# Optimization experiments

Hardware: AMD Instinct MI355X
Metric: run time of the kernel (lower is better)

Reference implementation:

```python
import jax, jax.numpy as jnp
import numpy as np

N = 20000          # nodes
E = 320000         # edges (avg degree 16)
D_IN, D1, D2, D_OUT = 256, 512, 256, 64
EPS = 1e-5


def _glorot(key, shape):
    lim = (6.0 / (shape[0] + shape[1])) ** 0.5
    return jax.random.uniform(key, shape, jnp.float32, -lim, lim)


def setup_inputs() -> dict:
    key = jax.random.key(0)
    ks = jax.random.split(key, 8)
    x = jax.random.normal(ks[0], (N, D_IN), jnp.float32)
    edge_index = jax.random.randint(ks[1], (2, E), 0, N, dtype=jnp.int64)
    return {
        "x": x,
        "edge_index": edge_index,
        # SAGEConv 1 (SoftmaxAggregation temperature t1 over inp_dim channels)
        "t1": jnp.ones((1, D_IN), jnp.float32),
        "Wl1": _glorot(ks[2], (D_IN, D1)), "bl1": jnp.zeros((D1,), jnp.float32),
        "Wr1": _glorot(ks[3], (D_IN, D1)),
        "g1": jnp.ones((D1,), jnp.float32), "beta1": jnp.zeros((D1,), jnp.float32),
        # SAGEConv 2
        "t2": jnp.ones((1, D1), jnp.float32),
        "Wl2": _glorot(ks[4], (D1, D2)), "bl2": jnp.zeros((D2,), jnp.float32),
        "Wr2": _glorot(ks[5], (D1, D2)),
        "g2": jnp.ones((D2,), jnp.float32), "beta2": jnp.zeros((D2,), jnp.float32),
        # final linear + LayerNorm
        "Wf": _glorot(ks[6], (D2, D_OUT)), "bf": jnp.zeros((D_OUT,), jnp.float32),
        "gx": jnp.ones((D_OUT,), jnp.float32), "betax": jnp.zeros((D_OUT,), jnp.float32),
    }


def _sage_softmax(x, src, dst, t, Wl, bl, Wr, n):
    """SAGEConv with learnable per-channel SoftmaxAggregation."""
    m = x[src]                                              # [E, C] gathered messages
    a = m * t                                               # scaled logits
    amax = jax.ops.segment_max(a, dst, num_segments=n)      # [N, C]
    e = jnp.exp(a - amax[dst])
    denom = jax.ops.segment_sum(e, dst, num_segments=n)     # [N, C]
    w = e / denom[dst]                                      # segment softmax weights
    agg = jax.ops.segment_sum(m * w, dst, num_segments=n)   # weighted neighbor sum
    return agg @ Wl + bl + x @ Wr


def _graph_ln(x, g, b):
    # PyG LayerNorm mode='graph', batch=None: normalize over ALL nodes & channels
    mu = x.mean()
    std = jnp.sqrt(((x - mu) ** 2).mean())
    return (x - mu) / (std + EPS) * g + b


def _ln(x, g, b):
    mu = x.mean(-1, keepdims=True)
    var = ((x - mu) ** 2).mean(-1, keepdims=True)
    return (x - mu) / jnp.sqrt(var + EPS) * g + b


def reference(x, edge_index, t1, Wl1, bl1, Wr1, g1, beta1,
              t2, Wl2, bl2, Wr2, g2, beta2, Wf, bf, gx, betax):
    src, dst = edge_index[0], edge_index[1]
    h = _sage_softmax(x, src, dst, t1, Wl1, bl1, Wr1, N)
    h = jax.nn.relu(_graph_ln(h, g1, beta1))
    h = _sage_softmax(h, src, dst, t2, Wl2, bl2, Wr2, N)
    h = jax.nn.relu(_graph_ln(h, g2, beta2))
    p = h.mean(0, keepdims=True)                            # global_mean_pool, batch=None -> [1, 256]
    out = _ln(p @ Wf + bf, gx, betax)
    return jax.nn.relu(out)
```

## Files before the change

kernel.cpp:

```cpp
#include <hip/hip_runtime.h>
#include <math.h>

#define NODES 20000
#define MPAD  20096
#define EDGES 320000
#define EPSV  1e-5f
#define LOG2E 1.4426950408889634f

typedef short bf16x8 __attribute__((ext_vector_type(8)));
typedef float f32x4  __attribute__((ext_vector_type(4)));
typedef float f2     __attribute__((ext_vector_type(2)));

__device__ __forceinline__ unsigned short f2bf(float f) {
    unsigned int u = __float_as_uint(f);
    u = (u + 0x7fffu + ((u >> 16) & 1u)) >> 16;
    return (unsigned short)u;
}
__device__ __forceinline__ float bf2f(unsigned short h) {
    return __uint_as_float(((unsigned int)h) << 16);
}

__device__ __forceinline__ void load_lds16(const unsigned short* g, unsigned short* l) {
    __builtin_amdgcn_global_load_lds(
        (const __attribute__((address_space(1))) unsigned int*)g,
        (__attribute__((address_space(3))) unsigned int*)l, 16, 0, 0);
}

__global__ void k_count(const int* __restrict__ dst, int* __restrict__ counts) {
    int e = blockIdx.x * blockDim.x + threadIdx.x;
    if (e < EDGES) atomicAdd(&counts[dst[e]], 1);
}

__global__ void k_scan(const int* __restrict__ counts, int* __restrict__ offs) {
    __shared__ int ssum[256];
    int t = threadIdx.x;
    const int chunk = (NODES + 255) / 256;
    int b = t * chunk, e = b + chunk;
    if (b > NODES) b = NODES;
    if (e > NODES) e = NODES;
    int s = 0;
    for (int i = b; i < e; i++) s += counts[i];
    ssum[t] = s;
    __syncthreads();
    int v = s;
#pragma unroll
    for (int o = 1; o < 256; o <<= 1) {
        int add = (t >= o) ? ssum[t - o] : 0;
        __syncthreads();
        v += add;
        ssum[t] = v;
        __syncthreads();
    }
    int run = v - s;
    if (t == 255) offs[NODES] = v;
    for (int i = b; i < e; i++) { offs[i] = run; run += counts[i]; }
}

__global__ void k_scatter(const int* __restrict__ src, const int* __restrict__ dst,
                          const int* __restrict__ offs, int* __restrict__ cursor,
                          int* __restrict__ csr_src) {
    int e = blockIdx.x * blockDim.x + threadIdx.x;
    if (e < EDGES) {
        int d = dst[e];
        int pos = atomicAdd(&cursor[d], 1);
        csr_src[offs[d] + pos] = src[e];
    }
}

__global__ void k_cast(const float* __restrict__ in, unsigned short* __restrict__ out) {
    int i = (blockIdx.x * blockDim.x + threadIdx.x) * 4;
    float4 v = *(const float4*)(in + i);
    out[i + 0] = f2bf(v.x); out[i + 1] = f2bf(v.y);
    out[i + 2] = f2bf(v.z); out[i + 3] = f2bf(v.w);
}

__global__ void k_transpose_all(const float* __restrict__ Wl1, const float* __restrict__ Wr1,
                                const float* __restrict__ Wl2, const float* __restrict__ Wr2,
                                unsigned short* __restrict__ o1l, unsigned short* __restrict__ o1r,
                                unsigned short* __restrict__ o2l, unsigned short* __restrict__ o2r) {
    __shared__ float tile[32][33];
    int z = blockIdx.z;
    const float* W = (z == 0) ? Wl1 : (z == 1) ? Wr1 : (z == 2) ? Wl2 : Wr2;
    unsigned short* Wt = (z == 0) ? o1l : (z == 1) ? o1r : (z == 2) ? o2l : o2r;
    int K = (z < 2) ? 256 : 512, N = (z < 2) ? 512 : 256;
    int nb = N / 32;
    int n0 = (blockIdx.x % nb) * 32, k0 = (blockIdx.x / nb) * 32;
    int tx = threadIdx.x, ty = threadIdx.y;
#pragma unroll
    for (int j = 0; j < 4; j++)
        tile[ty + j * 8][tx] = W[(size_t)(k0 + ty + j * 8) * N + n0 + tx];
    __syncthreads();
#pragma unroll
    for (int j = 0; j < 4; j++)
        Wt[(size_t)(n0 + ty + j * 8) * K + k0 + tx] = f2bf(tile[tx][ty + j * 8]);
}

template <int C, int S, int UNR>
__global__ void k_agg(const unsigned short* __restrict__ xb, const float* __restrict__ tt,
                      const int* __restrict__ offs, const int* __restrict__ csr,
                      unsigned short* __restrict__ out) {
    constexpr int CS  = C / S;
    constexpr int VPL = CS / 64;
    constexpr int W   = VPL / 2;
    typedef unsigned int uv __attribute__((ext_vector_type(W)));
    typedef unsigned short usv __attribute__((ext_vector_type(VPL)));
    int waveg = (int)((blockIdx.x * (unsigned)blockDim.x + threadIdx.x) >> 6);
    int lane = threadIdx.x & 63;
    int node = waveg / S;
    int slice = waveg % S;
    if (node >= NODES) return;
    int beg = __builtin_amdgcn_readfirstlane(offs[node]);
    int end = __builtin_amdgcn_readfirstlane(offs[node + 1]);
    int cb = slice * CS + lane * VPL;
    const unsigned short* __restrict__ xcb = xb + cb;
    f2 tl[W], l[W], s[W];
#pragma unroll
    for (int i = 0; i < W; i++) {
        tl[i][0] = tt[cb + 2 * i] * LOG2E;
        tl[i][1] = tt[cb + 2 * i + 1] * LOG2E;
        l[i][0] = 0.f; l[i][1] = 0.f;
        s[i][0] = 0.f; s[i][1] = 0.f;
    }
    int k = beg;
    for (; k + UNR <= end; k += UNR) {
        uv v[UNR];
#pragma unroll
        for (int u = 0; u < UNR; u++) {
            int sn = csr[k + u];
            v[u] = *(const uv*)(xcb + (size_t)sn * C);
        }
#pragma unroll
        for (int u = 0; u < UNR; u++)
#pragma unroll
            for (int i = 0; i < W; i++) {
                unsigned wd = v[u][i];
                f2 xv;
                xv[0] = __uint_as_float(wd << 16);
                xv[1] = __uint_as_float(wd & 0xffff0000u);
                f2 a = xv * tl[i];
                f2 p;
                p[0] = __builtin_amdgcn_exp2f(a[0]);
                p[1] = __builtin_amdgcn_exp2f(a[1]);
                l[i] += p;
                s[i] = __builtin_elementwise_fma(p, xv, s[i]);
            }
    }
    for (; k < end; k++) {
        int sn = csr[k];
        uv vv = *(const uv*)(xcb + (size_t)sn * C);
#pragma unroll
        for (int i = 0; i < W; i++) {
            unsigned wd = vv[i];
            f2 xv;
            xv[0] = __uint_as_float(wd << 16);
            xv[1] = __uint_as_float(wd & 0xffff0000u);
            f2 a = xv * tl[i];
            f2 p;
            p[0] = __builtin_amdgcn_exp2f(a[0]);
            p[1] = __builtin_amdgcn_exp2f(a[1]);
            l[i] += p;
            s[i] = __builtin_elementwise_fma(p, xv, s[i]);
        }
    }
    bool has = end > beg;
    usv o;
#pragma unroll
    for (int i = 0; i < W; i++) {
        o[2 * i]     = f2bf(has ? s[i][0] / l[i][0] : 0.f);
        o[2 * i + 1] = f2bf(has ? s[i][1] / l[i][1] : 0.f);
    }
    *(usv*)(out + (size_t)node * C + cb) = o;
}

template <int K, int NT>
__global__ __launch_bounds__(256) void k_gemm_mfma(
    const unsigned short* __restrict__ A1, const unsigned short* __restrict__ B1t,
    const unsigned short* __restrict__ A2, const unsigned short* __restrict__ B2t,
    const float* __restrict__ bias, unsigned short* __restrict__ Co, int M,
    float* __restrict__ stat) {
    __shared__ short As[128 * 32];
    __shared__ short Bs[128 * 32];
    __shared__ float rs[256], rq[256];

    int t = threadIdx.x;
    int m0 = blockIdx.x * 128, n0 = blockIdx.y * 128;
    int wv = t >> 6, lane = t & 63;
    int wm = wv & 1, wn = wv >> 1;
    int lm = lane & 15, quad = lane >> 4;
    int sr = t >> 2;
    int sc8 = (t & 3) * 8;

    f32x4 acc[4][4] = {};

    for (int ph = 0; ph < 2; ph++) {
        const unsigned short* __restrict__ A  = ph ? A2 : A1;
        const unsigned short* __restrict__ Bt = ph ? B2t : B1t;
        for (int k0 = 0; k0 < K; k0 += 32) {
#pragma unroll
            for (int it = 0; it < 2; it++) {
                load_lds16(A  + (size_t)(m0 + it * 64 + sr) * K + k0 + sc8,
                           (unsigned short*)&As[it * 2048 + wv * 512]);
                load_lds16(Bt + (size_t)(n0 + it * 64 + sr) * K + k0 + sc8,
                           (unsigned short*)&Bs[it * 2048 + wv * 512]);
            }
            __syncthreads();
            bf16x8 af[4], bfr[4];
#pragma unroll
            for (int i = 0; i < 4; i++) {
                af[i]  = *(const bf16x8*)&As[(wm * 64 + i * 16 + lm) * 32 + quad * 8];
                bfr[i] = *(const bf16x8*)&Bs[(wn * 64 + i * 16 + lm) * 32 + quad * 8];
            }
#pragma unroll
            for (int mi = 0; mi < 4; mi++)
#pragma unroll
                for (int nj = 0; nj < 4; nj++)
                    acc[mi][nj] = __builtin_amdgcn_mfma_f32_16x16x32_bf16(
                        af[mi], bfr[nj], acc[mi][nj], 0, 0, 0);
            __syncthreads();
        }
    }

    float sum = 0.f, ss = 0.f;
#pragma unroll
    for (int mi = 0; mi < 4; mi++) {
        int rb = m0 + wm * 64 + mi * 16 + quad * 4;
#pragma unroll
        for (int nj = 0; nj < 4; nj++) {
            int col = n0 + wn * 64 + nj * 16 + lm;
            float bb = bias[col];
#pragma unroll
            for (int rg = 0; rg < 4; rg++) {
                int row = rb + rg;
                if (row < M) {
                    float y = acc[mi][nj][rg] + bb;
                    Co[(size_t)row * NT + col] = f2bf(y);
                    sum += y; ss += y * y;
                }
            }
        }
    }
    rs[t] = sum; rq[t] = ss;
    __syncthreads();
    for (int o = 128; o > 0; o >>= 1) {
        if (t < o) { rs[t] += rs[t + o]; rq[t] += rq[t + o]; }
        __syncthreads();
    }
    if (t == 0) { atomicAdd(&stat[0], rs[0]); atomicAdd(&stat[1], rq[0]); }
}

template <int C>
__global__ void k_ln_relu_b(unsigned short* __restrict__ h, int n,
                            const float* __restrict__ st,
                            const float* __restrict__ g, const float* __restrict__ b) {
    typedef unsigned short us8 __attribute__((ext_vector_type(8)));
    float mu = st[0] / (float)n;
    float var = st[1] / (float)n - mu * mu;
    var = var < 0.f ? 0.f : var;
    float inv = 1.0f / (sqrtf(var) + EPSV);
    int i8 = (blockIdx.x * blockDim.x + threadIdx.x) * 8;
    if (i8 >= n) return;
    int c = i8 & (C - 1);
    us8 v = *(const us8*)(h + i8);
    us8 o;
#pragma unroll
    for (int j = 0; j < 8; j++) {
        float y = (bf2f(v[j]) - mu) * inv * g[c + j] + b[c + j];
        o[j] = f2bf(fmaxf(y, 0.f));
    }
    *(us8*)(h + i8) = o;
}

__global__ void k_ln_colsum(const unsigned short* __restrict__ h, int n,
                            const float* __restrict__ st,
                            const float* __restrict__ g, const float* __restrict__ b,
                            float* __restrict__ colsum) {
    float mu = st[0] / (float)n;
    float var = st[1] / (float)n - mu * mu;
    var = var < 0.f ? 0.f : var;
    float inv = 1.0f / (sqrtf(var) + EPSV);
    int t = threadIdx.x;
    float gv = g[t], bv = b[t];
    float local = 0.f;
    int stride = gridDim.x * blockDim.x;
    for (int i = blockIdx.x * blockDim.x + t; i < n; i += stride) {
        float y = (bf2f(h[i]) - mu) * inv * gv + bv;
        local += fmaxf(y, 0.f);
    }
    atomicAdd(&colsum[t], local);
}

__global__ void k_final(const float* __restrict__ colsum, const float* __restrict__ Wf,
                        const float* __restrict__ bf, const float* __restrict__ gx,
                        const float* __restrict__ bx, float* __restrict__ out) {
    __shared__ float p[256];
    int t = threadIdx.x;
    p[t] = colsum[t] * (1.0f / (float)NODES);
    __syncthreads();
    if (t < 64) {
        float acc = bf[t];
        for (int c = 0; c < 256; c++) acc = fmaf(p[c], Wf[c * 64 + t], acc);
        float sum = acc;
        for (int o = 32; o > 0; o >>= 1) sum += __shfl_xor(sum, o);
        float mu = sum * (1.0f / 64.0f);
        float d = acc - mu;
        float vs = d * d;
        for (int o = 32; o > 0; o >>= 1) vs += __shfl_xor(vs, o);
        float var = vs * (1.0f / 64.0f);
        float y = d * rsqrtf(var + EPSV) * gx[t] + bx[t];
        out[t] = fmaxf(y, 0.f);
    }
}

extern "C" void kernel_launch(void* const* d_in, const int* in_sizes, int n_in,
                              void* d_out, int out_size, void* d_ws, size_t ws_size,
                              hipStream_t stream) {
    const float* x   = (const float*)d_in[0];
    const int*   ei  = (const int*)d_in[1];
    const float* t1  = (const float*)d_in[2];
    const float* Wl1 = (const float*)d_in[3];
    const float* bl1 = (const float*)d_in[4];
    const float* Wr1 = (const float*)d_in[5];
    const float* g1  = (const float*)d_in[6];
    const float* be1 = (const float*)d_in[7];
    const float* t2  = (const float*)d_in[8];
    const float* Wl2 = (const float*)d_in[9];
    const float* bl2 = (const float*)d_in[10];
    const float* Wr2 = (const float*)d_in[11];
    const float* g2  = (const float*)d_in[12];
    const float* be2 = (const float*)d_in[13];
    const float* Wf  = (const float*)d_in[14];
    const float* bf  = (const float*)d_in[15];
    const float* gx  = (const float*)d_in[16];
    const float* bx  = (const float*)d_in[17];
    float* out = (float*)d_out;

    char* ws = (char*)d_ws;
    size_t off = 0;
    auto alloc = [&](size_t bytes) { size_t o = off; off = (off + bytes + 511) & ~511ull; return o; };
    size_t o_counts = alloc((size_t)NODES * 4);
    size_t o_cursor = alloc((size_t)NODES * 4);
    size_t o_acc    = alloc(4 * 4);
    size_t o_colsum = alloc(256 * 4);
    size_t zero_bytes = off;
    size_t o_offs = alloc((size_t)(NODES + 1) * 4);
    size_t o_csrc = alloc((size_t)EDGES * 4);
    size_t o_w1l  = alloc((size_t)512 * 256 * 2);
    size_t o_w1r  = alloc((size_t)512 * 256 * 2);
    size_t o_w2l  = alloc((size_t)256 * 512 * 2);
    size_t o_w2r  = alloc((size_t)256 * 512 * 2);
    size_t o_bufX = alloc((size_t)MPAD * 256 * 2);
    size_t o_agg  = alloc((size_t)MPAD * 512 * 2);
    size_t o_h1   = alloc((size_t)MPAD * 512 * 2);

    int*   counts = (int*)(ws + o_counts);
    int*   cursor = (int*)(ws + o_cursor);
    float* acc    = (float*)(ws + o_acc);
    float* colsum = (float*)(ws + o_colsum);
    int*   offs   = (int*)(ws + o_offs);
    int*   csrc   = (int*)(ws + o_csrc);
    unsigned short* w1lt = (unsigned short*)(ws + o_w1l);
    unsigned short* w1rt = (unsigned short*)(ws + o_w1r);
    unsigned short* w2lt = (unsigned short*)(ws + o_w2l);
    unsigned short* w2rt = (unsigned short*)(ws + o_w2r);
    unsigned short* xb   = (unsigned short*)(ws + o_bufX);
    unsigned short* h2p  = (unsigned short*)(ws + o_bufX);
    unsigned short* aggb = (unsigned short*)(ws + o_agg);
    unsigned short* h1   = (unsigned short*)(ws + o_h1);

    const int* src = ei;
    const int* dst = ei + EDGES;

    hipMemsetAsync(ws, 0, zero_bytes, stream);

    k_count<<<(EDGES + 255) / 256, 256, 0, stream>>>(dst, counts);
    k_scan<<<1, 256, 0, stream>>>(counts, offs);
    k_scatter<<<(EDGES + 255) / 256, 256, 0, stream>>>(src, dst, offs, cursor, csrc);
    k_cast<<<NODES * 256 / 4 / 256, 256, 0, stream>>>(x, xb);
    k_transpose_all<<<dim3(128, 1, 4), dim3(32, 8), 0, stream>>>(
        Wl1, Wr1, Wl2, Wr2, w1lt, w1rt, w2lt, w2rt);

    k_agg<256, 2, 8><<<(NODES * 2 + 3) / 4, 256, 0, stream>>>(xb, t1, offs, csrc, aggb);
    k_gemm_mfma<256, 512><<<dim3(MPAD / 128, 4), 256, 0, stream>>>(
        aggb, w1lt, xb, w1rt, bl1, h1, NODES, acc);
    k_ln_relu_b<512><<<NODES * 512 / 8 / 256, 256, 0, stream>>>(h1, NODES * 512, acc, g1, be1);

    k_agg<512, 2, 4><<<(NODES * 2 + 3) / 4, 256, 0, stream>>>(h1, t2, offs, csrc, aggb);
    k_gemm_mfma<512, 256><<<dim3(MPAD / 128, 2), 256, 0, stream>>>(
        aggb, w2lt, h1, w2rt, bl2, h2p, NODES, acc + 2);
    k_ln_colsum<<<1024, 256, 0, stream>>>(h2p, NODES * 256, acc + 2, g2, be2, colsum);

    k_final<<<1, 256, 0, stream>>>(colsum, Wf, bf, gx, bx, out);
}
```

Baseline: 353.6 us.

## Fuse all GNN stages into one persistent cooperative kernel with grid syncs

Replaces the chain of separate kernel launches (CSR build, cast, transpose, two aggregation/GEMM/LN layers, final pooling) with a single cooperative persistent kernel whose stages are separated by grid-wide barriers. The GEMM tiles are reordered in groups of eight M-tiles, and the CSR scatter now counts down the per-node counters instead of using a separate cursor array. The intent is to cut per-launch overhead and inter-kernel gaps. The cost is grid-sync overhead, a grid capped at 1024 blocks with work looped over it, and possible register or occupancy pressure from packing every stage into one kernel.

```diff
diff --git a/kernel.cpp b/kernel.cpp
--- a/kernel.cpp
+++ b/kernel.cpp
@@ -1,5 +1,8 @@
 #include <hip/hip_runtime.h>
+#include <hip/hip_cooperative_groups.h>
 #include <math.h>
+
+namespace cg = cooperative_groups;
 
 #define NODES 20000
 #define MPAD  20096
@@ -26,368 +29,388 @@
         (__attribute__((address_space(3))) unsigned int*)l, 16, 0, 0);
 }
 
-__global__ void k_count(const int* __restrict__ dst, int* __restrict__ counts) {
-    int e = blockIdx.x * blockDim.x + threadIdx.x;
-    if (e < EDGES) atomicAdd(&counts[dst[e]], 1);
-}
-
-__global__ void k_scan(const int* __restrict__ counts, int* __restrict__ offs) {
-    __shared__ int ssum[256];
-    int t = threadIdx.x;
-    const int chunk = (NODES + 255) / 256;
-    int b = t * chunk, e = b + chunk;
-    if (b > NODES) b = NODES;
-    if (e > NODES) e = NODES;
-    int s = 0;
-    for (int i = b; i < e; i++) s += counts[i];
-    ssum[t] = s;
-    __syncthreads();
-    int v = s;
-#pragma unroll
-    for (int o = 1; o < 256; o <<= 1) {
-        int add = (t >= o) ? ssum[t - o] : 0;
-        __syncthreads();
-        v += add;
-        ssum[t] = v;
-        __syncthreads();
-    }
-    int run = v - s;
-    if (t == 255) offs[NODES] = v;
-    for (int i = b; i < e; i++) { offs[i] = run; run += counts[i]; }
-}
-
-__global__ void k_scatter(const int* __restrict__ src, const int* __restrict__ dst,
-                          const int* __restrict__ offs, int* __restrict__ cursor,
-                          int* __restrict__ csr_src) {
-    int e = blockIdx.x * blockDim.x + threadIdx.x;
-    if (e < EDGES) {
-        int d = dst[e];
-        int pos = atomicAdd(&cursor[d], 1);
-        csr_src[offs[d] + pos] = src[e];
-    }
-}
-
-__global__ void k_cast(const float* __restrict__ in, unsigned short* __restrict__ out) {
-    int i = (blockIdx.x * blockDim.x + threadIdx.x) * 4;
-    float4 v = *(const float4*)(in + i);
-    out[i + 0] = f2bf(v.x); out[i + 1] = f2bf(v.y);
-    out[i + 2] = f2bf(v.z); out[i + 3] = f2bf(v.w);
-}
-
-__global__ void k_transpose_all(const float* __restrict__ Wl1, const float* __restrict__ Wr1,
-                                const float* __restrict__ Wl2, const float* __restrict__ Wr2,
-                                unsigned short* __restrict__ o1l, unsigned short* __restrict__ o1r,
-                                unsigned short* __restrict__ o2l, unsigned short* __restrict__ o2r) {
-    __shared__ float tile[32][33];
-    int z = blockIdx.z;
-    const float* W = (z == 0) ? Wl1 : (z == 1) ? Wr1 : (z == 2) ? Wl2 : Wr2;
-    unsigned short* Wt = (z == 0) ? o1l : (z == 1) ? o1r : (z == 2) ? o2l : o2r;
-    int K = (z < 2) ? 256 : 512, N = (z < 2) ? 512 : 256;
-    int nb = N / 32;
-    int n0 = (blockIdx.x % nb) * 32, k0 = (blockIdx.x / nb) * 32;
-    int tx = threadIdx.x, ty = threadIdx.y;
-#pragma unroll
-    for (int j = 0; j < 4; j++)
-        tile[ty + j * 8][tx] = W[(size_t)(k0 + ty + j * 8) * N + n0 + tx];
-    __syncthreads();
-#pragma unroll
-    for (int j = 0; j < 4; j++)
-        Wt[(size_t)(n0 + ty + j * 8) * K + k0 + tx] = f2bf(tile[tx][ty + j * 8]);
-}
+union SMem {
+    struct { short As[128 * 32]; short Bs[128 * 32]; float rs[256]; float rq[256]; } g;
+    float tile[32][33];
+    int   ssum[256];
+    float p[256];
+};
+
+struct Params {
+    const int *src, *dst;
+    const float *x;
+    const float *t1, *bl1, *g1, *be1;
+    const float *t2, *bl2, *g2, *be2;
+    const float *Wl1, *Wr1, *Wl2, *Wr2;
+    const float *Wf, *bf, *gx, *bx;
+    float* out;
+    int *counts, *offs, *csrc;
+    float *acc, *colsum;
+    unsigned short *w1lt, *w1rt, *w2lt, *w2rt;
+    unsigned short *xb, *aggb, *h1, *h2p;
+};
 
 template <int C, int S, int UNR>
-__global__ void k_agg(const unsigned short* __restrict__ xb, const float* __restrict__ tt,
-                      const int* __restrict__ offs, const int* __restrict__ csr,
-                      unsigned short* __restrict__ out) {
+__device__ __forceinline__ void agg_phase(const unsigned short* __restrict__ xb,
+                                          const float* __restrict__ tt,
+                                          const int* __restrict__ offs,
+                                          const int* __restrict__ csr,
+                                          unsigned short* __restrict__ out,
+                                          int gwave, int nwaves) {
     constexpr int CS  = C / S;
     constexpr int VPL = CS / 64;
     constexpr int W   = VPL / 2;
     typedef unsigned int uv __attribute__((ext_vector_type(W)));
     typedef unsigned short usv __attribute__((ext_vector_type(VPL)));
-    int waveg = (int)((blockIdx.x * (unsigned)blockDim.x + threadIdx.x) >> 6);
     int lane = threadIdx.x & 63;
-    int node = waveg / S;
-    int slice = waveg % S;
-    if (node >= NODES) return;
-    int beg = __builtin_amdgcn_readfirstlane(offs[node]);
-    int end = __builtin_amdgcn_readfirstlane(offs[node + 1]);
-    int cb = slice * CS + lane * VPL;
-    const unsigned short* __restrict__ xcb = xb + cb;
-    f2 tl[W], l[W], s[W];
-#pragma unroll
-    for (int i = 0; i < W; i++) {
-        tl[i][0] = tt[cb + 2 * i] * LOG2E;
-        tl[i][1] = tt[cb + 2 * i + 1] * LOG2E;
-        l[i][0] = 0.f; l[i][1] = 0.f;
-        s[i][0] = 0.f; s[i][1] = 0.f;
-    }
-    int k = beg;
-    for (; k + UNR <= end; k += UNR) {
-        uv v[UNR];
-#pragma unroll
-        for (int u = 0; u < UNR; u++) {
-            int sn = csr[k + u];
-            v[u] = *(const uv*)(xcb + (size_t)sn * C);
-        }
-#pragma unroll
-        for (int u = 0; u < UNR; u++)
+    for (int wt = gwave; wt < NODES * S; wt += nwaves) {
+        int node = wt / S, slice = wt % S;
+        int beg = __builtin_amdgcn_readfirstlane(offs[node]);
+        int end = __builtin_amdgcn_readfirstlane(offs[node + 1]);
+        int cb = slice * CS + lane * VPL;
+        const unsigned short* __restrict__ xcb = xb + cb;
+        f2 tl[W], l[W], s[W];
+#pragma unroll
+        for (int i = 0; i < W; i++) {
+            tl[i][0] = tt[cb + 2 * i] * LOG2E;
+            tl[i][1] = tt[cb + 2 * i + 1] * LOG2E;
+            l[i][0] = 0.f; l[i][1] = 0.f;
+            s[i][0] = 0.f; s[i][1] = 0.f;
+        }
+        int k = beg;
+        for (; k + UNR <= end; k += UNR) {
+            uv v[UNR];
+#pragma unroll
+            for (int u = 0; u < UNR; u++) {
+                int sn = csr[k + u];
+                v[u] = *(const uv*)(xcb + (size_t)sn * C);
+            }
+#pragma unroll
+            for (int u = 0; u < UNR; u++)
+#pragma unroll
+                for (int i = 0; i < W; i++) {
+                    unsigned wd = v[u][i];
+                    f2 xv;
+                    xv[0] = __uint_as_float(wd << 16);
+                    xv[1] = __uint_as_float(wd & 0xffff0000u);
+                    f2 a = xv * tl[i];
+                    f2 pp;
+                    pp[0] = __builtin_amdgcn_exp2f(a[0]);
+                    pp[1] = __builtin_amdgcn_exp2f(a[1]);
+                    l[i] += pp;
+                    s[i] = __builtin_elementwise_fma(pp, xv, s[i]);
+                }
+        }
+        for (; k < end; k++) {
+            int sn = csr[k];
+            uv vv = *(const uv*)(xcb + (size_t)sn * C);
 #pragma unroll
             for (int i = 0; i < W; i++) {
-                unsigned wd = v[u][i];
+                unsigned wd = vv[i];
                 f2 xv;
                 xv[0] = __uint_as_float(wd << 16);
                 xv[1] = __uint_as_float(wd & 0xffff0000u);
                 f2 a = xv * tl[i];
-                f2 p;
-                p[0] = __builtin_amdgcn_exp2f(a[0]);
-                p[1] = __builtin_amdgcn_exp2f(a[1]);
-                l[i] += p;
-                s[i] = __builtin_elementwise_fma(p, xv, s[i]);
+                f2 pp;
+                pp[0] = __builtin_amdgcn_exp2f(a[0]);
+                pp[1] = __builtin_amdgcn_exp2f(a[1]);
+                l[i] += pp;
+                s[i] = __builtin_elementwise_fma(pp, xv, s[i]);
             }
-    }
-    for (; k < end; k++) {
-        int sn = csr[k];
-        uv vv = *(const uv*)(xcb + (size_t)sn * C);
+        }
+        bool has = end > beg;
+        usv o;
 #pragma unroll
         for (int i = 0; i < W; i++) {
-            unsigned wd = vv[i];
-            f2 xv;
-            xv[0] = __uint_as_float(wd << 16);
-            xv[1] = __uint_as_float(wd & 0xffff0000u);
-            f2 a = xv * tl[i];
-            f2 p;
-            p[0] = __builtin_amdgcn_exp2f(a[0]);
-            p[1] = __builtin_amdgcn_exp2f(a[1]);
-            l[i] += p;
-            s[i] = __builtin_elementwise_fma(p, xv, s[i]);
-        }
-    }
-    bool has = end > beg;
-    usv o;
-#pragma unroll
-    for (int i = 0; i < W; i++) {
-        o[2 * i]     = f2bf(has ? s[i][0] / l[i][0] : 0.f);
-        o[2 * i + 1] = f2bf(has ? s[i][1] / l[i][1] : 0.f);
-    }
-    *(usv*)(out + (size_t)node * C + cb) = o;
-}
-
-template <int K, int NT>
-__global__ __launch_bounds__(256) void k_gemm_mfma(
+            o[2 * i]     = f2bf(has ? s[i][0] / l[i][0] : 0.f);
+            o[2 * i + 1] = f2bf(has ? s[i][1] / l[i][1] : 0.f);
+        }
+        *(usv*)(out + (size_t)node * C + cb) = o;
+    }
+}
+
+template <int K, int NT, int NTILES>
+__device__ __forceinline__ void gemm_phase(SMem& sm,
     const unsigned short* __restrict__ A1, const unsigned short* __restrict__ B1t,
     const unsigned short* __restrict__ A2, const unsigned short* __restrict__ B2t,
     const float* __restrict__ bias, unsigned short* __restrict__ Co, int M,
     float* __restrict__ stat) {
-    __shared__ short As[128 * 32];
-    __shared__ short Bs[128 * 32];
-    __shared__ float rs[256], rq[256];
-
     int t = threadIdx.x;
-    int m0 = blockIdx.x * 128, n0 = blockIdx.y * 128;
-    int wv = t >> 6, lane = t & 63;
-    int wm = wv & 1, wn = wv >> 1;
-    int lm = lane & 15, quad = lane >> 4;
-    int sr = t >> 2;
-    int sc8 = (t & 3) * 8;
-
-    f32x4 acc[4][4] = {};
-
-    for (int ph = 0; ph < 2; ph++) {
-        const unsigned short* __restrict__ A  = ph ? A2 : A1;
-        const unsigned short* __restrict__ Bt = ph ? B2t : B1t;
-        for (int k0 = 0; k0 < K; k0 += 32) {
-#pragma unroll
-            for (int it = 0; it < 2; it++) {
-                load_lds16(A  + (size_t)(m0 + it * 64 + sr) * K + k0 + sc8,
-                           (unsigned short*)&As[it * 2048 + wv * 512]);
-                load_lds16(Bt + (size_t)(n0 + it * 64 + sr) * K + k0 + sc8,
-                           (unsigned short*)&Bs[it * 2048 + wv * 512]);
+    int G = gridDim.x;
+    constexpr int MH = 20;
+    for (int bx = blockIdx.x; bx < 8 * NTILES * MH; bx += G) {
+        int xid = bx & 7, q = bx >> 3;
+        int n = q % NTILES, mh = q / NTILES;
+        int m = mh * 8 + xid;
+        if (m * 128 >= MPAD) continue;
+        int m0 = m * 128, n0 = n * 128;
+        int wv = t >> 6, lane = t & 63;
+        int wm = wv & 1, wn = wv >> 1;
+        int lm = lane & 15, quad = lane >> 4;
+        int sr = t >> 2;
+        int sc8 = (t & 3) * 8;
+        f32x4 acc[4][4] = {};
+        __syncthreads();
+        for (int ph = 0; ph < 2; ph++) {
+            const unsigned short* __restrict__ A  = ph ? A2 : A1;
+            const unsigned short* __restrict__ Bt = ph ? B2t : B1t;
+            for (int k0 = 0; k0 < K; k0 += 32) {
+#pragma unroll
+                for (int it = 0; it < 2; it++) {
+                    load_lds16(A  + (size_t)(m0 + it * 64 + sr) * K + k0 + sc8,
+                               (unsigned short*)&sm.g.As[it * 2048 + wv * 512]);
+                    load_lds16(Bt + (size_t)(n0 + it * 64 + sr) * K + k0 + sc8,
+                               (unsigned short*)&sm.g.Bs[it * 2048 + wv * 512]);
+                }
+                __syncthreads();
+                bf16x8 af[4], bfr[4];
+#pragma unroll
+                for (int i = 0; i < 4; i++) {
+                    af[i]  = *(const bf16x8*)&sm.g.As[(wm * 64 + i * 16 + lm) * 32 + quad * 8];
+                    bfr[i] = *(const bf16x8*)&sm.g.Bs[(wn * 64 + i * 16 + lm) * 32 + quad * 8];
+                }
+#pragma unroll
+                for (int mi = 0; mi < 4; mi++)
+#pragma unroll
+                    for (int nj = 0; nj < 4; nj++)
+                        acc[mi][nj] = __builtin_amdgcn_mfma_f32_16x16x32_bf16(
+                            af[mi], bfr[nj], acc[mi][nj], 0, 0, 0);
+                __syncthreads();
             }
-            __syncthreads();
-            bf16x8 af[4], bfr[4];
-#pragma unroll
-            for (int i = 0; i < 4; i++) {
-                af[i]  = *(const bf16x8*)&As[(wm * 64 + i * 16 + lm) * 32 + quad * 8];
-                bfr[i] = *(const bf16x8*)&Bs[(wn * 64 + i * 16 + lm) * 32 + quad * 8];
-            }
-#pragma unroll
-            for (int mi = 0; mi < 4; mi++)
-#pragma unroll
-                for (int nj = 0; nj < 4; nj++)
-                    acc[mi][nj] = __builtin_amdgcn_mfma_f32_16x16x32_bf16(
-                        af[mi], bfr[nj], acc[mi][nj], 0, 0, 0);
-            __syncthreads();
-        }
-    }
-
-    float sum = 0.f, ss = 0.f;
-#pragma unroll
-    for (int mi = 0; mi < 4; mi++) {
-        int rb = m0 + wm * 64 + mi * 16 + quad * 4;
-#pragma unroll
-        for (int nj = 0; nj < 4; nj++) {
-            int col = n0 + wn * 64 + nj * 16 + lm;
-            float bb = bias[col];
-#pragma unroll
-            for (int rg = 0; rg < 4; rg++) {
-                int row = rb + rg;
-                if (row < M) {
-                    float y = acc[mi][nj][rg] + bb;
-                    Co[(size_t)row * NT + col] = f2bf(y);
-                    sum += y; ss += y * y;
+        }
+        float sum = 0.f, ss = 0.f;
+#pragma unroll
+        for (int mi = 0; mi < 4; mi++) {
+            int rb = m0 + wm * 64 + mi * 16 + quad * 4;
+#pragma unroll
+            for (int nj = 0; nj < 4; nj++) {
+                int col = n0 + wn * 64 + nj * 16 + lm;
+                float bb = bias[col];
+#pragma unroll
+                for (int rg = 0; rg < 4; rg++) {
+                    int row = rb + rg;
+                    if (row < M) {
+                        float y = acc[mi][nj][rg] + bb;
+                        Co[(size_t)row * NT + col] = f2bf(y);
+                        sum += y; ss += y * y;
+                    }
                 }
             }
         }
-    }
-    rs[t] = sum; rq[t] = ss;
-    __syncthreads();
-    for (int o = 128; o > 0; o >>= 1) {
-        if (t < o) { rs[t] += rs[t + o]; rq[t] += rq[t + o]; }
-        __syncthreads();
-    }
-    if (t == 0) { atomicAdd(&stat[0], rs[0]); atomicAdd(&stat[1], rq[0]); }
-}
-
-template <int C>
-__global__ void k_ln_relu_b(unsigned short* __restrict__ h, int n,
-                            const float* __restrict__ st,
-                            const float* __restrict__ g, const float* __restrict__ b) {
-    typedef unsigned short us8 __attribute__((ext_vector_type(8)));
-    float mu = st[0] / (float)n;
-    float var = st[1] / (float)n - mu * mu;
-    var = var < 0.f ? 0.f : var;
-    float inv = 1.0f / (sqrtf(var) + EPSV);
-    int i8 = (blockIdx.x * blockDim.x + threadIdx.x) * 8;
-    if (i8 >= n) return;
-    int c = i8 & (C - 1);
-    us8 v = *(const us8*)(h + i8);
-    us8 o;
-#pragma unroll
-    for (int j = 0; j < 8; j++) {
-        float y = (bf2f(v[j]) - mu) * inv * g[c + j] + b[c + j];
-        o[j] = f2bf(fmaxf(y, 0.f));
-    }
-    *(us8*)(h + i8) = o;
-}
-
-__global__ void k_ln_colsum(const unsigned short* __restrict__ h, int n,
-                            const float* __restrict__ st,
-                            const float* __restrict__ g, const float* __restrict__ b,
-                            float* __restrict__ colsum) {
-    float mu = st[0] / (float)n;
-    float var = st[1] / (float)n - mu * mu;
-    var = var < 0.f ? 0.f : var;
-    float inv = 1.0f / (sqrtf(var) + EPSV);
+        sm.g.rs[t] = sum; sm.g.rq[t] = ss;
+        __syncthreads();
+        for (int o = 128; o > 0; o >>= 1) {
+            if (t < o) { sm.g.rs[t] += sm.g.rs[t + o]; sm.g.rq[t] += sm.g.rq[t + o]; }
+            __syncthreads();
+        }
+        if (t == 0) { atomicAdd(&stat[0], sm.g.rs[0]); atomicAdd(&stat[1], sm.g.rq[0]); }
+    }
+}
+
+__global__ __launch_bounds__(256, 4) void k_mega(Params p) {
+    cg::grid_group gg = cg::this_grid();
+    __shared__ SMem sm;
     int t = threadIdx.x;
-    float gv = g[t], bv = b[t];
-    float local = 0.f;
-    int stride = gridDim.x * blockDim.x;
-    for (int i = blockIdx.x * blockDim.x + t; i < n; i += stride) {
-        float y = (bf2f(h[i]) - mu) * inv * gv + bv;
-        local += fmaxf(y, 0.f);
-    }
-    atomicAdd(&colsum[t], local);
-}
-
-__global__ void k_final(const float* __restrict__ colsum, const float* __restrict__ Wf,
-                        const float* __restrict__ bf, const float* __restrict__ gx,
-                        const float* __restrict__ bx, float* __restrict__ out) {
-    __shared__ float p[256];
-    int t = threadIdx.x;
-    p[t] = colsum[t] * (1.0f / (float)NODES);
-    __syncthreads();
-    if (t < 64) {
-        float acc = bf[t];
-        for (int c = 0; c < 256; c++) acc = fmaf(p[c], Wf[c * 64 + t], acc);
-        float sum = acc;
-        for (int o = 32; o > 0; o >>= 1) sum += __shfl_xor(sum, o);
-        float mu = sum * (1.0f / 64.0f);
-        float d = acc - mu;
-        float vs = d * d;
-        for (int o = 32; o > 0; o >>= 1) vs += __shfl_xor(vs, o);
-        float var = vs * (1.0f / 64.0f);
-        float y = d * rsqrtf(var + EPSV) * gx[t] + bx[t];
-        out[t] = fmaxf(y, 0.f);
+    int bid = blockIdx.x;
+    int G = gridDim.x;
+    int T = G * 256;
+    int gtid = bid * 256 + t;
+    int gwave = gtid >> 6;
+    int nwaves = T >> 6;
+
+    for (int i = gtid; i < NODES; i += T) p.counts[i] = 0;
+    if (bid == 0) { if (t < 4) p.acc[t] = 0.f; p.colsum[t] = 0.f; }
+    gg.sync();
+
+    for (int e = gtid; e < EDGES; e += T) atomicAdd(&p.counts[p.dst[e]], 1);
+    for (int i = gtid; i < NODES * 256 / 4; i += T) {
+        float4 v = *(const float4*)(p.x + (size_t)i * 4);
+        unsigned short* o = p.xb + (size_t)i * 4;
+        o[0] = f2bf(v.x); o[1] = f2bf(v.y); o[2] = f2bf(v.z); o[3] = f2bf(v.w);
+    }
+    for (int zz = bid; zz < 512; zz += G) {
+        int z = zz >> 7, idx = zz & 127;
+        const float* W = (z == 0) ? p.Wl1 : (z == 1) ? p.Wr1 : (z == 2) ? p.Wl2 : p.Wr2;
+        unsigned short* Wt = (z == 0) ? p.w1lt : (z == 1) ? p.w1rt : (z == 2) ? p.w2lt : p.w2rt;
+        int K = (z < 2) ? 256 : 512, N = (z < 2) ? 512 : 256;
+        int nb = N / 32;
+        int n0 = (idx % nb) * 32, k0 = (idx / nb) * 32;
+        int tx = t & 31, ty = t >> 5;
+        __syncthreads();
+#pragma unroll
+        for (int j = 0; j < 4; j++)
+            sm.tile[ty + j * 8][tx] = W[(size_t)(k0 + ty + j * 8) * N + n0 + tx];
+        __syncthreads();
+#pragma unroll
+        for (int j = 0; j < 4; j++)
+            Wt[(size_t)(n0 + ty + j * 8) * K + k0 + tx] = f2bf(sm.tile[tx][ty + j * 8]);
+    }
+    gg.sync();
+
+    if (bid == 0) {
+        const int chunk = (NODES + 255) / 256;
+        int b = t * chunk, e = b + chunk;
+        if (b > NODES) b = NODES;
+        if (e > NODES) e = NODES;
+        int s = 0;
+        for (int i = b; i < e; i++) s += p.counts[i];
+        sm.ssum[t] = s;
+        __syncthreads();
+        int v = s;
+#pragma unroll
+        for (int o = 1; o < 256; o <<= 1) {
+            int add = (t >= o) ? sm.ssum[t - o] : 0;
+            __syncthreads();
+            v += add;
+            sm.ssum[t] = v;
+            __syncthreads();
+        }
+        int run = v - s;
+        if (t == 255) p.offs[NODES] = v;
+        for (int i = b; i < e; i++) { p.offs[i] = run; run += p.counts[i]; }
+    }
+    gg.sync();
+
+    for (int e = gtid; e < EDGES; e += T) {
+        int d = p.dst[e];
+        int pos = atomicAdd(&p.counts[d], -1) - 1;
+        p.csrc[p.offs[d] + pos] = p.src[e];
+    }
+    gg.sync();
+
+    agg_phase<256, 2, 8>(p.xb, p.t1, p.offs, p.csrc, p.aggb, gwave, nwaves);
+    gg.sync();
+
+    gemm_phase<256, 512, 4>(sm, p.aggb, p.w1lt, p.xb, p.w1rt, p.bl1, p.h1, NODES, p.acc);
+    gg.sync();
+
+    {
+        typedef unsigned short us8 __attribute__((ext_vector_type(8)));
+        const float invn = 1.f / (float)(NODES * 512);
+        float mu = p.acc[0] * invn;
+        float var = p.acc[1] * invn - mu * mu;
+        var = var < 0.f ? 0.f : var;
+        float inv = 1.f / (sqrtf(var) + EPSV);
+        for (int i8 = gtid; i8 < NODES * 512 / 8; i8 += T) {
+            int i = i8 * 8;
+            int c = i & 511;
+            us8 v = *(const us8*)(p.h1 + i);
+            us8 o;
+#pragma unroll
+            for (int j = 0; j < 8; j++) {
+                float y = (bf2f(v[j]) - mu) * inv * p.g1[c + j] + p.be1[c + j];
+                o[j] = f2bf(fmaxf(y, 0.f));
+            }
+            *(us8*)(p.h1 + i) = o;
+        }
+    }
+    gg.sync();
+
+    agg_phase<512, 2, 4>(p.h1, p.t2, p.offs, p.csrc, p.aggb, gwave, nwaves);
+    gg.sync();
+
+    gemm_phase<512, 256, 2>(sm, p.aggb, p.w2lt, p.h1, p.w2rt, p.bl2, p.h2p, NODES, p.acc + 2);
+    gg.sync();
+
+    {
+        int nb9 = G < 512 ? G : 512;
+        if (bid < nb9) {
+            const int n = NODES * 256;
+            const float invn = 1.f / (float)n;
+            float mu = p.acc[2] * invn;
+            float var = p.acc[3] * invn - mu * mu;
+            var = var < 0.f ? 0.f : var;
+            float inv = 1.f / (sqrtf(var) + EPSV);
+            float gv = p.g2[t], bv = p.be2[t];
+            float local = 0.f;
+            for (int i = bid * 256 + t; i < n; i += nb9 * 256)
+                local += fmaxf((bf2f(p.h2p[i]) - mu) * inv * gv + bv, 0.f);
+            atomicAdd(&p.colsum[t], local);
+        }
+    }
+    gg.sync();
+
+    if (bid == 0) {
+        sm.p[t] = p.colsum[t] * (1.0f / (float)NODES);
+        __syncthreads();
+        if (t < 64) {
+            float acc = p.bf[t];
+            for (int c = 0; c < 256; c++) acc = fmaf(sm.p[c], p.Wf[c * 64 + t], acc);
+            float sum = acc;
+            for (int o = 32; o > 0; o >>= 1) sum += __shfl_xor(sum, o);
+            float mu = sum * (1.0f / 64.0f);
+            float d = acc - mu;
+            float vs = d * d;
+            for (int o = 32; o > 0; o >>= 1) vs += __shfl_xor(vs, o);
+            float var = vs * (1.0f / 64.0f);
+            float y = d * rsqrtf(var + EPSV) * p.gx[t] + p.bx[t];
+            p.out[t] = fmaxf(y, 0.f);
+        }
     }
 }
 
 extern "C" void kernel_launch(void* const* d_in, const int* in_sizes, int n_in,
                               void* d_out, int out_size, void* d_ws, size_t ws_size,
                               hipStream_t stream) {
-    const float* x   = (const float*)d_in[0];
-    const int*   ei  = (const int*)d_in[1];
-    const float* t1  = (const float*)d_in[2];
-    const float* Wl1 = (const float*)d_in[3];
-    const float* bl1 = (const float*)d_in[4];
-    const float* Wr1 = (const float*)d_in[5];
-    const float* g1  = (const float*)d_in[6];
-    const float* be1 = (const float*)d_in[7];
-    const float* t2  = (const float*)d_in[8];
-    const float* Wl2 = (const float*)d_in[9];
-    const float* bl2 = (const float*)d_in[10];
-    const float* Wr2 = (const float*)d_in[11];
-    const float* g2  = (const float*)d_in[12];
-    const float* be2 = (const float*)d_in[13];
-    const float* Wf  = (const float*)d_in[14];
-    const float* bf  = (const float*)d_in[15];
-    const float* gx  = (const float*)d_in[16];
-    const float* bx  = (const float*)d_in[17];
-    float* out = (float*)d_out;
+    const int* ei = (const int*)d_in[1];
 
     char* ws = (char*)d_ws;
     size_t off = 0;
     auto alloc = [&](size_t bytes) { size_t o = off; off = (off + bytes + 511) & ~511ull; return o; };
     size_t o_counts = alloc((size_t)NODES * 4);
-    size_t o_cursor = alloc((size_t)NODES * 4);
     size_t o_acc    = alloc(4 * 4);
     size_t o_colsum = alloc(256 * 4);
-    size_t zero_bytes = off;
-    size_t o_offs = alloc((size_t)(NODES + 1) * 4);
-    size_t o_csrc = alloc((size_t)EDGES * 4);
-    size_t o_w1l  = alloc((size_t)512 * 256 * 2);
-    size_t o_w1r  = alloc((size_t)512 * 256 * 2);
-    size_t o_w2l  = alloc((size_t)256 * 512 * 2);
-    size_t o_w2r  = alloc((size_t)256 * 512 * 2);
-    size_t o_bufX = alloc((size_t)MPAD * 256 * 2);
-    size_t o_agg  = alloc((size_t)MPAD * 512 * 2);
-    size_t o_h1   = alloc((size_t)MPAD * 512 * 2);
-
-    int*   counts = (int*)(ws + o_counts);
-    int*   cursor = (int*)(ws + o_cursor);
-    float* acc    = (float*)(ws + o_acc);
-    float* colsum = (float*)(ws + o_colsum);
-    int*   offs   = (int*)(ws + o_offs);
-    int*   csrc   = (int*)(ws + o_csrc);
-    unsigned short* w1lt = (unsigned short*)(ws + o_w1l);
-    unsigned short* w1rt = (unsigned short*)(ws + o_w1r);
-    unsigned short* w2lt = (unsigned short*)(ws + o_w2l);
-    unsigned short* w2rt = (unsigned short*)(ws + o_w2r);
-    unsigned short* xb   = (unsigned short*)(ws + o_bufX);
-    unsigned short* h2p  = (unsigned short*)(ws + o_bufX);
-    unsigned short* aggb = (unsigned short*)(ws + o_agg);
-    unsigned short* h1   = (unsigned short*)(ws + o_h1);
-
-    const int* src = ei;
-    const int* dst = ei + EDGES;
-
-    hipMemsetAsync(ws, 0, zero_bytes, stream);
-
-    k_count<<<(EDGES + 255) / 256, 256, 0, stream>>>(dst, counts);
-    k_scan<<<1, 256, 0, stream>>>(counts, offs);
-    k_scatter<<<(EDGES + 255) / 256, 256, 0, stream>>>(src, dst, offs, cursor, csrc);
-    k_cast<<<NODES * 256 / 4 / 256, 256, 0, stream>>>(x, xb);
-    k_transpose_all<<<dim3(128, 1, 4), dim3(32, 8), 0, stream>>>(
-        Wl1, Wr1, Wl2, Wr2, w1lt, w1rt, w2lt, w2rt);
-
-    k_agg<256, 2, 8><<<(NODES * 2 + 3) / 4, 256, 0, stream>>>(xb, t1, offs, csrc, aggb);
-    k_gemm_mfma<256, 512><<<dim3(MPAD / 128, 4), 256, 0, stream>>>(
-        aggb, w1lt, xb, w1rt, bl1, h1, NODES, acc);
-    k_ln_relu_b<512><<<NODES * 512 / 8 / 256, 256, 0, stream>>>(h1, NODES * 512, acc, g1, be1);
-
-    k_agg<512, 2, 4><<<(NODES * 2 + 3) / 4, 256, 0, stream>>>(h1, t2, offs, csrc, aggb);
-    k_gemm_mfma<512, 256><<<dim3(MPAD / 128, 2), 256, 0, stream>>>(
-        aggb, w2lt, h1, w2rt, bl2, h2p, NODES, acc + 2);
-    k_ln_colsum<<<1024, 256, 0, stream>>>(h2p, NODES * 256, acc + 2, g2, be2, colsum);
-
-    k_final<<<1, 256, 0, stream>>>(colsum, Wf, bf, gx, bx, out);
-}
+    size_t o_offs   = alloc((size_t)(NODES + 1) * 4);
+    size_t o_csrc   = alloc((size_t)EDGES * 4);
+    size_t o_w1l    = alloc((size_t)512 * 256 * 2);
+    size_t o_w1r    = alloc((size_t)512 * 256 * 2);
+    size_t o_w2l    = alloc((size_t)256 * 512 * 2);
+    size_t o_w2r    = alloc((size_t)256 * 512 * 2);
+    size_t o_bufX   = alloc((size_t)MPAD * 256 * 2);
+    size_t o_agg    = alloc((size_t)MPAD * 512 * 2);
+    size_t o_h1     = alloc((size_t)(MPAD + 512) * 512 * 2);
+
+    Params p;
+    p.src = ei;
+    p.dst = ei + EDGES;
+    p.x   = (const float*)d_in[0];
+    p.t1  = (const float*)d_in[2];
+    p.Wl1 = (const float*)d_in[3];
+    p.bl1 = (const float*)d_in[4];
+    p.Wr1 = (const float*)d_in[5];
+    p.g1  = (const float*)d_in[6];
+    p.be1 = (const float*)d_in[7];
+    p.t2  = (const float*)d_in[8];
+    p.Wl2 = (const float*)d_in[9];
+    p.bl2 = (const float*)d_in[10];
+    p.Wr2 = (const float*)d_in[11];
+    p.g2  = (const float*)d_in[12];
+    p.be2 = (const float*)d_in[13];
+    p.Wf  = (const float*)d_in[14];
+    p.bf  = (const float*)d_in[15];
+    p.gx  = (const float*)d_in[16];
+    p.bx  = (const float*)d_in[17];
+    p.out = (float*)d_out;
+    p.counts = (int*)(ws + o_counts);
+    p.offs   = (int*)(ws + o_offs);
+    p.csrc   = (int*)(ws + o_csrc);
+    p.acc    = (float*)(ws + o_acc);
+    p.colsum = (float*)(ws + o_colsum);
+    p.w1lt = (unsigned short*)(ws + o_w1l);
+    p.w1rt = (unsigned short*)(ws + o_w1r);
+    p.w2lt = (unsigned short*)(ws + o_w2l);
+    p.w2rt = (unsigned short*)(ws + o_w2r);
+    p.xb   = (unsigned short*)(ws + o_bufX);
+    p.h2p  = (unsigned short*)(ws + o_bufX);
+    p.aggb = (unsigned short*)(ws + o_agg);
+    p.h1   = (unsigned short*)(ws + o_h1);
+
+    int nb = 0;
+    if (hipOccupancyMaxActiveBlocksPerMultiprocessor(&nb, k_mega, 256, 0) != hipSuccess || nb < 1)
+        nb = 2;
+    int G = nb * 256;
+    if (G > 1024) G = 1024;
+
+    void* args[] = { &p };
+    hipLaunchCooperativeKernel((const void*)k_mega, dim3(G), dim3(256), args, 0, stream);
+}
```

New measurement: 1.100 ms. 3.11x slower.
